# Kernel optimization log

Measured on AMD Instinct MI355X. Metric: run time of the kernel, lower is better.

Reference implementation:

```python
import jax, jax.numpy as jnp
import numpy as np

# dims: L blocks, S cur_seq, M memory_len, B batch, D embed, H heads, IN input_dim
L, S, M, B, D, H, IN = 4, 512, 512, 8, 1024, 16, 128
HD = D // H
GRU_BIAS = 2.0  # config['gru_bias']


def _ln(x, s, b, eps=1e-5):
    mu = x.mean(-1, keepdims=True)
    var = ((x - mu) ** 2).mean(-1, keepdims=True)
    return (x - mu) * jax.lax.rsqrt(var + eps) * s + b


def _pos_emb(full_seq, dim):
    # SinusoidalPE: freqs = arange(0, dim, 2.0); inv = 10000**(-freqs/dim); seq descending
    freqs = jnp.arange(0, dim, 2.0)
    inv = 10000.0 ** (-freqs / dim)
    seq = jnp.arange(full_seq - 1, -1, -1.0)
    ang = seq[:, None] * inv[None, :]
    return jnp.concatenate([jnp.sin(ang), jnp.cos(ang)], axis=-1)  # (F, dim)


def _rel_shift(x):
    # x: (q, k, b, h) -> Transformer-XL relative shift
    q, k, b, h = x.shape
    xp = jnp.pad(x, ((0, 0), (1, 0), (0, 0), (0, 0)))
    return xp.reshape(k + 1, q, b, h)[1:].reshape(q, k, b, h)


def _gru(x, y, Wr, Ur, Wz, Uz, Wg, Ug):
    r = jax.nn.sigmoid(y @ Wr + x @ Ur)
    z = jax.nn.sigmoid(y @ Wz + x @ Uz - GRU_BIAS)
    hcand = jnp.tanh(y @ Wg + (r * x) @ Ug)
    return (1.0 - z) * x + z * hcand


def setup_inputs() -> dict:
    key = jax.random.key(0)
    ks = iter(jax.random.split(key, 64))

    def mat(*shape):
        return jax.random.normal(next(ks), shape, jnp.float32) * (shape[-2] ** -0.5)

    return dict(
        h=jax.random.normal(next(ks), (B, S, IN), jnp.float32),
        memory=jnp.zeros((L, M, B, D), jnp.float32),
        We=mat(IN, D), be=jnp.zeros((D,), jnp.float32),
        ln1_s=jnp.ones((L, D), jnp.float32), ln1_b=jnp.zeros((L, D), jnp.float32),
        ln2_s=jnp.ones((L, D), jnp.float32), ln2_b=jnp.zeros((L, D), jnp.float32),
        Wq=mat(L, D, D), bq=jnp.zeros((L, D), jnp.float32),
        Wk=mat(L, D, D), bk=jnp.zeros((L, D), jnp.float32),
        Wv=mat(L, D, D), bv=jnp.zeros((L, D), jnp.float32),
        Wr=mat(L, D, D), br=jnp.zeros((L, D), jnp.float32),
        Wo=mat(L, D, D), bo=jnp.zeros((L, D), jnp.float32),
        u=jax.random.normal(next(ks), (L, H, HD), jnp.float32) * 0.02,
        vb=jax.random.normal(next(ks), (L, H, HD), jnp.float32) * 0.02,
        gWr=mat(L, 2, D, D), gUr=mat(L, 2, D, D),
        gWz=mat(L, 2, D, D), gUz=mat(L, 2, D, D),
        gWg=mat(L, 2, D, D), gUg=mat(L, 2, D, D),
        fW1=mat(L, D, 4 * D), fb1=jnp.zeros((L, 4 * D), jnp.float32),
        fW2=mat(L, 4 * D, D), fb2=jnp.zeros((L, D), jnp.float32),
    )


def reference(h, memory, We, be, ln1_s, ln1_b, ln2_s, ln2_b,
              Wq, bq, Wk, bk, Wv, bv, Wr, br, Wo, bo, u, vb,
              gWr, gUr, gWz, gUz, gWg, gUg, fW1, fb1, fW2, fb2):
    x = jnp.transpose(h, (1, 0, 2))                      # (S, B, IN)
    x = jax.nn.gelu(x @ We + be, approximate=False)      # (S, B, D)
    F = S + M
    pos = _pos_emb(F, D)                                 # (F, D)
    mask = jnp.triu(jnp.ones((S, F), bool), k=1 + M)     # (S, F)
    scale = HD ** -0.5
    out = x
    for i in range(L):
        full = jnp.concatenate([memory[i], out], axis=0)  # (F, B, D)
        qn = _ln(out, ln1_s[i], ln1_b[i])
        kn = _ln(full, ln1_s[i], ln1_b[i])
        q = (qn @ Wq[i] + bq[i]).reshape(S, B, H, HD)
        k = (kn @ Wk[i] + bk[i]).reshape(F, B, H, HD)
        v = (kn @ Wv[i] + bv[i]).reshape(F, B, H, HD)
        r = (pos @ Wr[i] + br[i]).reshape(F, H, HD)
        content = jnp.einsum('ibhd,jbhd->ijbh', q + u[i], k)
        position = _rel_shift(jnp.einsum('ibhd,jhd->ijbh', q + vb[i], r))
        attn = (content + position) * scale               # (S, F, B, H)
        attn = jnp.where(mask[:, :, None, None], -1e30, attn)
        a = jax.nn.softmax(attn, axis=1)
        y = jnp.einsum('ijbh,jbhd->ibhd', a, v).reshape(S, B, D) @ Wo[i] + bo[i]
        y = jax.nn.gelu(y, approximate=False)
        out1 = _gru(out, y, gWr[i, 0], gUr[i, 0], gWz[i, 0], gUz[i, 0], gWg[i, 0], gUg[i, 0])
        e = _ln(out1, ln2_s[i], ln2_b[i])
        e = jax.nn.gelu(e @ fW1[i] + fb1[i], approximate=False)
        e = jax.nn.gelu(e @ fW2[i] + fb2[i], approximate=False)
        out = _gru(out1, e, gWr[i, 1], gUr[i, 1], gWz[i, 1], gUz[i, 1], gWg[i, 1], gUg[i, 1])
    return jnp.transpose(out, (1, 0, 2))                  # (B, S, D)
```

## Files before the change

### kernel.cpp

```cpp
#include <hip/hip_runtime.h>

typedef unsigned short u16;
typedef unsigned long long u64;
typedef __attribute__((ext_vector_type(8))) short bf16x8;
typedef __attribute__((ext_vector_type(4))) float f32x4;

#define DEVI __device__ __forceinline__

DEVI u16 f2b(float f) {
  unsigned u = __float_as_uint(f);
  u += 0x7fffu + ((u >> 16) & 1u);
  return (u16)(u >> 16);
}
DEVI float b2f(u16 v) { return __uint_as_float((unsigned)v << 16); }
DEVI float tanh_f(float x) {
  float xc = fminf(fmaxf(x, -15.f), 15.f);
  float e = __expf(2.f * xc);
  return (e - 1.f) / (e + 1.f);
}
DEVI float gelu_f(float x) {
  float u = 0.7978845608028654f * x * (1.f + 0.044715f * x * x);
  return 0.5f * x * (1.f + tanh_f(u));
}
DEVI float sigm_f(float x) { return 1.f / (1.f + __expf(-x)); }

DEVI void gload16(const void* g, void* l) {
  __builtin_amdgcn_global_load_lds((__attribute__((address_space(1))) void*)g,
                                   (__attribute__((address_space(3))) void*)l, 16, 0, 0);
}

__global__ __launch_bounds__(256) void gemm_bt(
    const u16* __restrict__ A, const u16* __restrict__ Bt,
    const float* __restrict__ bias, float* __restrict__ C32, u16* __restrict__ C16,
    int M, int N, int K, int ldA, int ldB, int ldC,
    long long sA, long long sBb, long long sBh, long long sC, int nH, int flags)
{
  __shared__ __align__(16) u16 Sm[2][256 * 64];
  const int z = blockIdx.z;
  const int zb = z / nH, zh = z - zb * nH;
  A  += (long long)z * sA;
  Bt += (long long)zb * sBb + (long long)zh * sBh;
  const long long cOff = (long long)z * sC;
  const int m0 = blockIdx.x * 128, n0 = blockIdx.y * 128;
  const int t = threadIdx.x, lane = t & 63;
  const int wm = ((t >> 7) & 1) * 64, wn = ((t >> 6) & 1) * 64;

  f32x4 acc[4][4];
#pragma unroll
  for (int i = 0; i < 4; ++i)
#pragma unroll
    for (int j = 0; j < 4; ++j) { f32x4 zz = {0.f, 0.f, 0.f, 0.f}; acc[i][j] = zz; }

  auto stage = [&](int buf, int k0) {
#pragma unroll
    for (int r = 0; r < 4; ++r) {
      const int c = r * 256 + t;
      const int row = c >> 3;
      const int col = (c & 7) << 3;
      int ga = m0 + row; if (ga >= M) ga = M - 1;
      gload16(A + (long long)ga * ldA + (k0 + col),
              &Sm[buf][(size_t)(r * 256 + (t & 192)) * 8]);
      int gb = n0 + row; if (gb >= N) gb = N - 1;
      gload16(Bt + (long long)gb * ldB + (k0 + col),
              &Sm[buf][(size_t)(1024 + r * 256 + (t & 192)) * 8]);
    }
  };

  auto compute = [&](int buf) {
    const u16* As = &Sm[buf][0];
    const u16* Bs = &Sm[buf][128 * 64];
#pragma unroll
    for (int ks = 0; ks < 2; ++ks) {
      const int ko = ks * 32 + ((lane >> 4) << 3);
      bf16x8 af[4], bfv[4];
#pragma unroll
      for (int i = 0; i < 4; ++i)
        af[i] = *(const bf16x8*)&As[(wm + i * 16 + (lane & 15)) * 64 + ko];
#pragma unroll
      for (int i = 0; i < 4; ++i)
        bfv[i] = *(const bf16x8*)&Bs[(wn + i * 16 + (lane & 15)) * 64 + ko];
#pragma unroll
      for (int mi = 0; mi < 4; ++mi)
#pragma unroll
        for (int ni = 0; ni < 4; ++ni)
          acc[mi][ni] = __builtin_amdgcn_mfma_f32_16x16x32_bf16(af[mi], bfv[ni], acc[mi][ni], 0, 0, 0);
    }
  };

  stage(0, 0);
  __syncthreads();
  int cur = 0;
  for (int k0 = 64; k0 < K; k0 += 64) {
    stage(cur ^ 1, k0);
    compute(cur);
    __syncthreads();
    cur ^= 1;
  }
  compute(cur);

  const int cb = n0 + wn + (lane & 15);
  const int rb = m0 + wm + ((lane >> 4) << 2);
#pragma unroll
  for (int ni = 0; ni < 4; ++ni) {
    const int col = cb + ni * 16;
    if (col >= N) continue;
    const float bv = (flags & 2) ? bias[col] : 0.f;
#pragma unroll
    for (int mi = 0; mi < 4; ++mi) {
#pragma unroll
      for (int q = 0; q < 4; ++q) {
        const int row = rb + mi * 16 + q;
        if (row >= M) continue;
        float x = acc[mi][ni][q] + bv;
        if (flags & 1) x = gelu_f(x);
        long long o;
        if (flags & 16)
          o = ((long long)((row & 7) * 16 + (col >> 6)) * ldC + (row >> 3)) * 64 + (col & 63);
        else if (flags & 32)
          o = ((long long)(col >> 6) * 1024 + row) * 64 + (col & 63);
        else
          o = cOff + (long long)row * ldC + col;
        if (flags & 4) C32[o] = x;
        if (flags & 8) C16[o] = f2b(x);
      }
    }
  }
}

__global__ __launch_bounds__(256) void fused_attn(
    const u16* __restrict__ Qb,
    const u16* __restrict__ Kb,
    const u16* __restrict__ Vt,
    const u16* __restrict__ Rh,
    const float* __restrict__ uK,
    const float* __restrict__ vbR,
    u16* __restrict__ Y)
{
  constexpr int F = 1024;
  const int bid = blockIdx.x;
  const int wk = (bid & 7) * 128 + (bid >> 3);
  const int i0 = (wk & 7) * 64;
  const int bh = wk >> 3;
  const int h = bh & 15;

  __shared__ __align__(16) u16 Qs[64 * 64];
  __shared__ __align__(16) u16 Ks[64 * 64];
  __shared__ __align__(16) u16 Vs[64 * 64];
  __shared__ __align__(16) u16 Rs[2][64 * 64];
  __shared__ __align__(8) u16 PBT[128 * 68];
  __shared__ __align__(16) u16 Ps[4][16][72];
  __shared__ float uKs[64];
  __shared__ float vbRs[2][64];

  const int t = threadIdx.x;
  const int lane = t & 63;
  const int wq = t >> 6;
  const int l15 = lane & 15, lhi = lane >> 4;

  const u16* Qg = Qb + ((size_t)bh * 512 + i0) * 64;
  const u16* Kg = Kb + (size_t)bh * F * 64;
  const u16* Vg = Vt + (size_t)bh * 64 * F;
  const u16* Rg = Rh + (size_t)h * F * 64;
  const float* uKg = uK + (size_t)bh * F;
  const float* vbRg = vbR + (size_t)h * F;

  auto stageQ = [&]() {
#pragma unroll
    for (int rnd = 0; rnd < 2; ++rnd) {
      const int idx = rnd * 256 + t;
      const int row = idx >> 3;
      const int gs = (idx & 7) ^ (row & 7);
      gload16(Qg + row * 64 + gs * 8, Qs + (size_t)(rnd * 256 + (t & 192)) * 8);
    }
  };
  auto stageK = [&](int j0) {
#pragma unroll
    for (int rnd = 0; rnd < 2; ++rnd) {
      const int idx = rnd * 256 + t;
      const int row = idx >> 3;
      const int gs = (idx & 7) ^ (row & 7);
      gload16(Kg + (j0 + row) * 64 + gs * 8, Ks + (size_t)(rnd * 256 + (t & 192)) * 8);
    }
  };
  auto stageV = [&](int j0) {
#pragma unroll
    for (int rnd = 0; rnd < 2; ++rnd) {
      const int idx = rnd * 256 + t;
      const int row = idx >> 3;
      const int gs = (idx & 7) ^ (row & 7);
      gload16(Vg + row * F + j0 + gs * 8, Vs + (size_t)(rnd * 256 + (t & 192)) * 8);
    }
  };
  auto stageR = [&](u16* dst, int cbase) {
#pragma unroll
    for (int rnd = 0; rnd < 2; ++rnd) {
      const int idx = rnd * 256 + t;
      const int row = idx >> 3;
      const int gs = (idx & 7) ^ (row & 7);
      int grow = cbase + row; if (grow > 1023) grow = 1023;
      gload16(Rg + grow * 64 + gs * 8, dst + (size_t)(rnd * 256 + (t & 192)) * 8);
    }
  };

  stageQ();
  const int c_lo0 = 448 - i0;
  stageR(Rs[0], c_lo0);
  if (t < 64) {
    int c = c_lo0 + t; if (c > 1023) c = 1023;
    vbRs[0][t] = vbRg[c];
  }

  f32x4 Oacc[4];
#pragma unroll
  for (int i = 0; i < 4; ++i) { f32x4 zz = {0.f, 0.f, 0.f, 0.f}; Oacc[i] = zz; }
  float mrow[4] = {-3.0e38f, -3.0e38f, -3.0e38f, -3.0e38f};
  float lrow[4] = {0.f, 0.f, 0.f, 0.f};

  const int nT = i0 / 64 + 9;
  for (int st = 0; st < nT; ++st) {
    const int j0 = st * 64;
    const int c_hi = j0 - i0 + 512;
    const bool lastT = (st == nT - 1);
    __syncthreads();
    stageK(j0);
    stageV(j0);
    if (!lastT) stageR(Rs[(st + 1) & 1], c_hi);
    if (t < 64) uKs[t] = uKg[j0 + t];
    else if (t < 128 && !lastT) {
      int c = c_hi + (t - 64); if (c > 1023) c = 1023;
      vbRs[(st + 1) & 1][t - 64] = vbRg[c];
    }
    __syncthreads();

    const u16* RsLo = Rs[st & 1];
    const u16* RsHi = Rs[(st + 1) & 1];
    const float* vLo = vbRs[st & 1];
    const float* vHi = vbRs[(st + 1) & 1];

    f32x4 cacc[4], pbacc[8];
#pragma unroll
    for (int i = 0; i < 4; ++i) { f32x4 zz = {0.f, 0.f, 0.f, 0.f}; cacc[i] = zz; }
#pragma unroll
    for (int i = 0; i < 8; ++i) { f32x4 zz = {0.f, 0.f, 0.f, 0.f}; pbacc[i] = zz; }
    __builtin_amdgcn_s_setprio(1);
#pragma unroll
    for (int ks = 0; ks < 2; ++ks) {
      const int arow = wq * 16 + l15;
      const bf16x8 a = *(const bf16x8*)&Qs[arow * 64 + (((ks * 4 + lhi) ^ (arow & 7)) << 3)];
#pragma unroll
      for (int ni = 0; ni < 4; ++ni) {
        const int brow = ni * 16 + l15;
        const bf16x8 bk_ = *(const bf16x8*)&Ks[brow * 64 + (((ks * 4 + lhi) ^ (brow & 7)) << 3)];
        cacc[ni] = __builtin_amdgcn_mfma_f32_16x16x32_bf16(a, bk_, cacc[ni], 0, 0, 0);
      }
#pragma unroll
      for (int ni = 0; ni < 8; ++ni) {
        if (ni >= 4 && lastT) continue;
        const int brow = (ni & 3) * 16 + l15;
        const u16* rt = (ni < 4) ? RsLo : RsHi;
        const bf16x8 br_ = *(const bf16x8*)&rt[brow * 64 + (((ks * 4 + lhi) ^ (brow & 7)) << 3)];
        pbacc[ni] = __builtin_amdgcn_mfma_f32_16x16x32_bf16(a, br_, pbacc[ni], 0, 0, 0);
      }
    }
    __builtin_amdgcn_s_setprio(0);

#pragma unroll
    for (int ni = 0; ni < 8; ++ni) {
      if (ni >= 4 && lastT) continue;
      u64 w = (u64)f2b(pbacc[ni][0]) | ((u64)f2b(pbacc[ni][1]) << 16) |
              ((u64)f2b(pbacc[ni][2]) << 32) | ((u64)f2b(pbacc[ni][3]) << 48);
      *(u64*)&PBT[(size_t)(ni * 16 + l15) * 68 + wq * 16 + lhi * 4] = w;
    }

    const int lim = i0 - j0 + 512;
    float sc[4][4];
#pragma unroll
    for (int ni = 0; ni < 4; ++ni) {
      const int dj = ni * 16 + l15;
      const float uk = uKs[dj];
#pragma unroll
      for (int qq = 0; qq < 4; ++qq) {
        const int di = wq * 16 + lhi * 4 + qq;
        const int cc = dj - di + 63;
        const float pb = b2f(PBT[(size_t)cc * 68 + di]);
        const float vr = (cc < 64) ? vLo[cc] : vHi[cc - 64];
        float s = (cacc[ni][qq] + uk + pb + vr) * 0.125f;
        if (dj - di > lim) s = -1e30f;
        sc[ni][qq] = s;
      }
    }

    float nm[4], esc[4];
#pragma unroll
    for (int qq = 0; qq < 4; ++qq) {
      float r = fmaxf(fmaxf(sc[0][qq], sc[1][qq]), fmaxf(sc[2][qq], sc[3][qq]));
      r = fmaxf(r, __shfl_xor(r, 1));
      r = fmaxf(r, __shfl_xor(r, 2));
      r = fmaxf(r, __shfl_xor(r, 4));
      r = fmaxf(r, __shfl_xor(r, 8));
      nm[qq] = fmaxf(mrow[qq], r);
      esc[qq] = __expf(mrow[qq] - nm[qq]);
      mrow[qq] = nm[qq];
    }
    float ps[4][4];
    float rsum[4] = {0.f, 0.f, 0.f, 0.f};
#pragma unroll
    for (int ni = 0; ni < 4; ++ni)
#pragma unroll
      for (int qq = 0; qq < 4; ++qq) {
        float p = __expf(sc[ni][qq] - nm[qq]);
        ps[ni][qq] = p;
        rsum[qq] += p;
      }
#pragma unroll
    for (int qq = 0; qq < 4; ++qq) {
      float r = rsum[qq];
      r += __shfl_xor(r, 1);
      r += __shfl_xor(r, 2);
      r += __shfl_xor(r, 4);
      r += __shfl_xor(r, 8);
      lrow[qq] = lrow[qq] * esc[qq] + r;
    }
#pragma unroll
    for (int nd = 0; nd < 4; ++nd)
#pragma unroll
      for (int qq = 0; qq < 4; ++qq) Oacc[nd][qq] *= esc[qq];

#pragma unroll
    for (int ni = 0; ni < 4; ++ni)
#pragma unroll
      for (int qq = 0; qq < 4; ++qq)
        Ps[wq][lhi * 4 + qq][ni * 16 + l15] = f2b(ps[ni][qq]);
    __builtin_amdgcn_s_setprio(1);
#pragma unroll
    for (int ks = 0; ks < 2; ++ks) {
      const bf16x8 pa = *(const bf16x8*)&Ps[wq][l15][ks * 32 + lhi * 8];
#pragma unroll
      for (int nd = 0; nd < 4; ++nd) {
        const int vrow = nd * 16 + l15;
        const bf16x8 vb_ = *(const bf16x8*)&Vs[vrow * 64 + (((ks * 4 + lhi) ^ (vrow & 7)) << 3)];
        Oacc[nd] = __builtin_amdgcn_mfma_f32_16x16x32_bf16(pa, vb_, Oacc[nd], 0, 0, 0);
      }
    }
    __builtin_amdgcn_s_setprio(0);
  }

  float inv[4];
#pragma unroll
  for (int qq = 0; qq < 4; ++qq) inv[qq] = 1.f / lrow[qq];
  const int b = bh >> 4;
#pragma unroll
  for (int nd = 0; nd < 4; ++nd)
#pragma unroll
    for (int qq = 0; qq < 4; ++qq) {
      const int row = i0 + wq * 16 + lhi * 4 + qq;
      const int d = nd * 16 + l15;
      Y[(size_t)row * 8192 + b * 1024 + h * 64 + d] = f2b(Oacc[nd][qq] * inv[qq]);
    }
}

__global__ __launch_bounds__(256) void uk_kernel(const u16* __restrict__ Kb,
                                                 const float* __restrict__ u,
                                                 float* __restrict__ uK)
{
  const long long idx = (long long)blockIdx.x * 256 + threadIdx.x;
  const int h = (int)((idx >> 10) & 15);
  const u16* k = Kb + idx * 64;
  const float* uh = u + h * 64;
  float s = 0.f;
#pragma unroll
  for (int j = 0; j < 8; ++j) {
    bf16x8 kv = *(const bf16x8*)&k[j * 8];
#pragma unroll
    for (int e = 0; e < 8; ++e) s += b2f((u16)kv[e]) * uh[j * 8 + e];
  }
  uK[idx] = s;
}

__global__ __launch_bounds__(256) void vbr_kernel(const u16* __restrict__ Rh,
                                                  const float* __restrict__ vb,
                                                  float* __restrict__ vbR)
{
  const long long idx = (long long)blockIdx.x * 256 + threadIdx.x;
  const int h = (int)(idx >> 10);
  const u16* r = Rh + idx * 64;
  const float* vh = vb + h * 64;
  float s = 0.f;
#pragma unroll
  for (int j = 0; j < 8; ++j) {
    bf16x8 rv = *(const bf16x8*)&r[j * 8];
#pragma unroll
    for (int e = 0; e < 8; ++e) s += b2f((u16)rv[e]) * vh[j * 8 + e];
  }
  vbR[idx] = s;
}

#define MAXW 20
struct WPack {
  const float* src[MAXW];
  u16* dst[MAXW];
  int K[MAXW], N[MAXW];
  int tilePrefix[MAXW + 1];
  int nm;
};

__global__ __launch_bounds__(256) void wtrans_kernel(WPack p) {
  int bid = blockIdx.x;
  int m = 0;
  while (m < p.nm && bid >= p.tilePrefix[m + 1]) ++m;
  if (m >= p.nm) return;
  const int lt = bid - p.tilePrefix[m];
  const int K = p.K[m], N = p.N[m];
  const int tN = N >> 5;
  const int kt = lt / tN, nt = lt - kt * tN;
  const int k0 = kt << 5, n0 = nt << 5;
  const float* src = p.src[m];
  u16* dst = p.dst[m];
  __shared__ float tile[32][33];
  const int t = threadIdx.x;
  const int r = t >> 3, c4 = (t & 7) << 2;
  float4 v = *(const float4*)&src[(size_t)(k0 + r) * N + n0 + c4];
  tile[r][c4 + 0] = v.x; tile[r][c4 + 1] = v.y; tile[r][c4 + 2] = v.z; tile[r][c4 + 3] = v.w;
  __syncthreads();
  u16 o0 = f2b(tile[c4 + 0][r]);
  u16 o1 = f2b(tile[c4 + 1][r]);
  u16 o2 = f2b(tile[c4 + 2][r]);
  u16 o3 = f2b(tile[c4 + 3][r]);
  u64 w = (u64)o0 | ((u64)o1 << 16) | ((u64)o2 << 32) | ((u64)o3 << 48);
  *(u64*)&dst[(size_t)(n0 + r) * K + k0 + c4] = w;
}

__global__ __launch_bounds__(256) void ln_kernel(
    const float* __restrict__ Xmem, const float* __restrict__ Xout, int rowsMem,
    const float* __restrict__ sc, const float* __restrict__ bi, u16* __restrict__ dst)
{
  const int row = blockIdx.x;
  const float* src = (row < rowsMem) ? (Xmem + (long long)row * 1024)
                                     : (Xout + (long long)(row - rowsMem) * 1024);
  const int t = threadIdx.x;
  float4 v = *(const float4*)&src[t * 4];
  float s1 = v.x + v.y + v.z + v.w;
  float s2 = v.x * v.x + v.y * v.y + v.z * v.z + v.w * v.w;
#pragma unroll
  for (int o = 32; o > 0; o >>= 1) { s1 += __shfl_down(s1, o); s2 += __shfl_down(s2, o); }
  __shared__ float red[8];
  const int wv = t >> 6;
  if ((t & 63) == 0) { red[wv * 2] = s1; red[wv * 2 + 1] = s2; }
  __syncthreads();
  s1 = red[0] + red[2] + red[4] + red[6];
  s2 = red[1] + red[3] + red[5] + red[7];
  const float mu = s1 * (1.f / 1024.f);
  const float var = s2 * (1.f / 1024.f) - mu * mu;
  const float rs = rsqrtf(var + 1e-5f);
  float vals[4] = {v.x, v.y, v.z, v.w};
  u16 o4[4];
#pragma unroll
  for (int j = 0; j < 4; ++j) {
    const int c = t * 4 + j;
    o4[j] = f2b((vals[j] - mu) * rs * sc[c] + bi[c]);
  }
  *(u64*)&dst[(long long)row * 1024 + t * 4] =
      (u64)o4[0] | ((u64)o4[1] << 16) | ((u64)o4[2] << 32) | ((u64)o4[3] << 48);
}

__global__ __launch_bounds__(256) void prep_vt16(const u16* __restrict__ Vf, u16* __restrict__ VT)
{
  const int f0 = blockIdx.x * 64;
  const int bh = blockIdx.y;
  const int b = bh >> 4, h = bh & 15;
  __shared__ u16 tl[64 * 64];
  const int t = threadIdx.x;
  {
    const int fr = t >> 2, c0 = (t & 3) * 16;
    const u16* src = Vf + ((size_t)(f0 + fr) * 8 + b) * 1024 + h * 64 + c0;
    *(bf16x8*)&tl[fr * 64 + c0] = *(const bf16x8*)src;
    *(bf16x8*)&tl[fr * 64 + c0 + 8] = *(const bf16x8*)(src + 8);
  }
  __syncthreads();
  {
    const int dr = t >> 2, c0 = (t & 3) * 16;
    u16* dst = VT + ((long long)bh * 64 + dr) * 1024 + f0 + c0;
#pragma unroll
    for (int j = 0; j < 16; ++j) dst[j] = tl[(c0 + j) * 64 + dr];
  }
}

__global__ __launch_bounds__(256) void pe_kernel(u16* __restrict__ PEB)
{
  const long long idx = (long long)blockIdx.x * 256 + threadIdx.x;
  const int p = (int)(idx >> 10);
  const int d = idx & 1023;
  const int q = d & 511;
  const float inv = powf(10000.f, -(float)(2 * q) * (1.f / 1024.f));
  const float ang = (float)(1023 - p) * inv;
  PEB[idx] = f2b((d < 512) ? sinf(ang) : cosf(ang));
}

__global__ __launch_bounds__(256) void embed_conv(const float* __restrict__ h, u16* __restrict__ A)
{
  const long long idx = (long long)blockIdx.x * 256 + threadIdx.x;
  const int c = idx & 127;
  const int r = (int)(idx >> 7);
  const int s = r >> 3, b = r & 7;
  A[idx] = f2b(h[(((long long)b * 512 + s) << 7) + c]);
}

__global__ __launch_bounds__(256) void gru_elemA(const float* __restrict__ T1, float* __restrict__ T2,
                                                 const float* __restrict__ X, u16* __restrict__ RXBF)
{
  const long long i4 = ((long long)blockIdx.x * 256 + threadIdx.x) * 4;
  const int row = (int)(i4 >> 10);
  const int c = i4 & 1023;
  const float* t1 = T1 + (long long)row * 3072 + c;
  float* t2 = T2 + (long long)row * 2048 + c;
  float4 ry = *(const float4*)t1;
  float4 zy = *(const float4*)(t1 + 1024);
  float4 rx = *(const float4*)t2;
  float4 zx = *(const float4*)(t2 + 1024);
  float4 x = *(const float4*)(X + i4);
  float rr[4], zz[4];
  rr[0] = sigm_f(ry.x + rx.x); rr[1] = sigm_f(ry.y + rx.y);
  rr[2] = sigm_f(ry.z + rx.z); rr[3] = sigm_f(ry.w + rx.w);
  zz[0] = sigm_f(zy.x + zx.x - 2.f); zz[1] = sigm_f(zy.y + zx.y - 2.f);
  zz[2] = sigm_f(zy.z + zx.z - 2.f); zz[3] = sigm_f(zy.w + zx.w - 2.f);
  u16 o4[4];
  o4[0] = f2b(rr[0] * x.x); o4[1] = f2b(rr[1] * x.y);
  o4[2] = f2b(rr[2] * x.z); o4[3] = f2b(rr[3] * x.w);
  *(u64*)&RXBF[i4] = (u64)o4[0] | ((u64)o4[1] << 16) | ((u64)o4[2] << 32) | ((u64)o4[3] << 48);
  float4 zo; zo.x = zz[0]; zo.y = zz[1]; zo.z = zz[2]; zo.w = zz[3];
  *(float4*)t2 = zo;
}

__global__ __launch_bounds__(256) void gru_elemB(const float* __restrict__ T1, const float* __restrict__ T2,
                                                 const float* __restrict__ TG, const float* __restrict__ X,
                                                 float* __restrict__ O, u16* __restrict__ XBF)
{
  const long long i4 = ((long long)blockIdx.x * 256 + threadIdx.x) * 4;
  const int row = (int)(i4 >> 10);
  const int c = i4 & 1023;
  float4 gy = *(const float4*)(T1 + (long long)row * 3072 + 2048 + c);
  float4 tt = *(const float4*)(TG + i4);
  float4 z = *(const float4*)(T2 + (long long)row * 2048 + c);
  float4 x = *(const float4*)(X + i4);
  float4 o;
  o.x = (1.f - z.x) * x.x + z.x * tanh_f(gy.x + tt.x);
  o.y = (1.f - z.y) * x.y + z.y * tanh_f(gy.y + tt.y);
  o.z = (1.f - z.z) * x.z + z.z * tanh_f(gy.z + tt.z);
  o.w = (1.f - z.w) * x.w + z.w * tanh_f(gy.w + tt.w);
  *(float4*)(O + i4) = o;
  u16 o4[4];
  o4[0] = f2b(o.x); o4[1] = f2b(o.y); o4[2] = f2b(o.z); o4[3] = f2b(o.w);
  *(u64*)&XBF[i4] = (u64)o4[0] | ((u64)o4[1] << 16) | ((u64)o4[2] << 32) | ((u64)o4[3] << 48);
}

__global__ __launch_bounds__(256) void out_transpose(const float* __restrict__ O, float* __restrict__ dst)
{
  const long long i4 = ((long long)blockIdx.x * 256 + threadIdx.x) * 4;
  const int d = i4 & 1023;
  const int r = (int)(i4 >> 10);
  const int s = r >> 3, b = r & 7;
  float4 v = *(const float4*)(O + i4);
  *(float4*)&dst[(((long long)b * 512 + s) << 10) + d] = v;
}

extern "C" void kernel_launch(void* const* d_in, const int* in_sizes, int n_in,
                              void* d_out, int out_size, void* d_ws, size_t ws_size,
                              hipStream_t stream)
{
  (void)in_sizes; (void)n_in; (void)out_size; (void)ws_size;
  const float* h_in   = (const float*)d_in[0];
  const float* memory = (const float*)d_in[1];
  const float* We     = (const float*)d_in[2];
  const float* be     = (const float*)d_in[3];
  const float* ln1s   = (const float*)d_in[4];
  const float* ln1b   = (const float*)d_in[5];
  const float* ln2s   = (const float*)d_in[6];
  const float* ln2b   = (const float*)d_in[7];
  const float* Wq     = (const float*)d_in[8];
  const float* bq     = (const float*)d_in[9];
  const float* Wk     = (const float*)d_in[10];
  const float* bk     = (const float*)d_in[11];
  const float* Wv     = (const float*)d_in[12];
  const float* bv     = (const float*)d_in[13];
  const float* Wr     = (const float*)d_in[14];
  const float* br     = (const float*)d_in[15];
  const float* Wo     = (const float*)d_in[16];
  const float* bo     = (const float*)d_in[17];
  const float* uu     = (const float*)d_in[18];
  const float* vbp    = (const float*)d_in[19];
  const float* gWr    = (const float*)d_in[20];
  const float* gUr    = (const float*)d_in[21];
  const float* gWz    = (const float*)d_in[22];
  const float* gUz    = (const float*)d_in[23];
  const float* gWg    = (const float*)d_in[24];
  const float* gUg    = (const float*)d_in[25];
  const float* fW1    = (const float*)d_in[26];
  const float* fb1    = (const float*)d_in[27];
  const float* fW2    = (const float*)d_in[28];
  const float* fb2    = (const float*)d_in[29];

  constexpr int S = 512, MM = 512, B = 8, D = 1024, H = 16, IN = 128, F = 1024;
  constexpr int SB = 4096, FB = 8192;
  constexpr long long DD = (long long)D * D;

  char* ws = (char*)d_ws;
  size_t off = 0;
  auto alloc = [&](size_t bytes) -> size_t {
    size_t o = off; off = (off + bytes + 255) & ~(size_t)255; return o;
  };
  const size_t oWT   = alloc((size_t)25 * DD * 2);
  const size_t oWET  = alloc((size_t)D * IN * 2);
  const size_t oPEB  = alloc((size_t)F * D * 2);
  const size_t oOUT  = alloc((size_t)SB * D * 4);
  const size_t oOUT1 = alloc((size_t)SB * D * 4);
  const size_t oXBF  = alloc((size_t)SB * D * 2);
  const size_t oYBF  = alloc((size_t)SB * D * 2);
  const size_t oYBFA = alloc((size_t)SB * D * 2);
  const size_t oABUF = alloc((size_t)SB * D * 2);
  const size_t oKN   = alloc((size_t)FB * D * 2);
  const size_t oQB   = alloc((size_t)B * H * S * 64 * 2);
  const size_t oKBH  = alloc((size_t)B * H * F * 64 * 2);
  const size_t oVT   = alloc((size_t)B * H * F * 64 * 2);
  const size_t oRH   = alloc((size_t)H * F * 64 * 2);
  const size_t oUK   = alloc((size_t)B * H * F * 4);
  const size_t oVBR  = alloc((size_t)H * F * 4);
  const size_t oUNI  = off;

  u16* WTp   = (u16*)(ws + oWT);
  u16* WETp  = (u16*)(ws + oWET);
  u16* PEBp  = (u16*)(ws + oPEB);
  float* OUTp  = (float*)(ws + oOUT);
  float* OUT1p = (float*)(ws + oOUT1);
  u16* XBFp  = (u16*)(ws + oXBF);
  u16* YBFp  = (u16*)(ws + oYBF);
  u16* YBFAp = (u16*)(ws + oYBFA);
  u16* ABUFp = (u16*)(ws + oABUF);
  u16* KNp   = (u16*)(ws + oKN);
  u16* QBp   = (u16*)(ws + oQB);
  u16* KBHp  = (u16*)(ws + oKBH);
  u16* VTp   = (u16*)(ws + oVT);
  u16* RHp   = (u16*)(ws + oRH);
  float* uKp  = (float*)(ws + oUK);
  float* vbRp = (float*)(ws + oVBR);
  u16* VF16p  = (u16*)(ws + oUNI);
  float* T1   = (float*)(ws + oUNI);
  float* T2   = (float*)(ws + oUNI + (size_t)SB * 3 * D * 4);
  float* TGp  = (float*)(ws + oUNI + (size_t)SB * 5 * D * 4);
  u16* FFNBp  = (u16*)(ws + oUNI);

  auto gemm = [&](const u16* A, const u16* Bt, const float* bias, float* C32, u16* C16,
                  int M, int N, int K, int ldA, int ldB, int ldC,
                  long long sA, long long sBb, long long sBh, long long sC, int nH, int Z,
                  int flags) {
    dim3 grid((M + 127) / 128, (N + 127) / 128, Z);
    gemm_bt<<<grid, 256, 0, stream>>>(A, Bt, bias, C32, C16, M, N, K, ldA, ldB, ldC,
                                      sA, sBb, sBh, sC, nH, flags);
  };

  pe_kernel<<<(F * D) / 256, 256, 0, stream>>>(PEBp);
  {
    WPack p{};
    p.nm = 1; p.src[0] = We; p.dst[0] = WETp; p.K[0] = IN; p.N[0] = D;
    p.tilePrefix[0] = 0; p.tilePrefix[1] = (IN / 32) * (D / 32);
    wtrans_kernel<<<p.tilePrefix[1], 256, 0, stream>>>(p);
  }
  embed_conv<<<(SB * IN) / 256, 256, 0, stream>>>(h_in, ABUFp);
  gemm(ABUFp, WETp, be, OUTp, XBFp, SB, D, IN, IN, IN, D, 0, 0, 0, 0, 1, 1, 1 | 2 | 4 | 8);

  for (int li = 0; li < 4; ++li) {
    WPack p{};
    int nt = 0, id = 0;
    auto addw = [&](const float* s, u16* d, int K, int N) {
      p.src[id] = s; p.dst[id] = d; p.K[id] = K; p.N[id] = N;
      p.tilePrefix[id] = nt; nt += (K / 32) * (N / 32); ++id;
    };
    addw(Wq + li * DD, WTp + 0 * DD, D, D);
    addw(Wk + li * DD, WTp + 1 * DD, D, D);
    addw(Wv + li * DD, WTp + 2 * DD, D, D);
    addw(Wr + li * DD, WTp + 3 * DD, D, D);
    addw(Wo + li * DD, WTp + 4 * DD, D, D);
    addw(gWr + (li * 2 + 0) * DD, WTp + 5 * DD, D, D);
    addw(gWz + (li * 2 + 0) * DD, WTp + 6 * DD, D, D);
    addw(gWg + (li * 2 + 0) * DD, WTp + 7 * DD, D, D);
    addw(gUr + (li * 2 + 0) * DD, WTp + 8 * DD, D, D);
    addw(gUz + (li * 2 + 0) * DD, WTp + 9 * DD, D, D);
    addw(gUg + (li * 2 + 0) * DD, WTp + 10 * DD, D, D);
    addw(gWr + (li * 2 + 1) * DD, WTp + 11 * DD, D, D);
    addw(gWz + (li * 2 + 1) * DD, WTp + 12 * DD, D, D);
    addw(gWg + (li * 2 + 1) * DD, WTp + 13 * DD, D, D);
    addw(gUr + (li * 2 + 1) * DD, WTp + 14 * DD, D, D);
    addw(gUz + (li * 2 + 1) * DD, WTp + 15 * DD, D, D);
    addw(gUg + (li * 2 + 1) * DD, WTp + 16 * DD, D, D);
    addw(fW1 + li * (long long)D * 4096, WTp + 17 * DD, D, 4096);
    addw(fW2 + li * (long long)4096 * D, WTp + 21 * DD, 4096, D);
    p.tilePrefix[id] = nt; p.nm = id;
    wtrans_kernel<<<nt, 256, 0, stream>>>(p);

    ln_kernel<<<FB, 256, 0, stream>>>(memory + (long long)li * MM * B * D, OUTp, MM * B,
                                      ln1s + li * D, ln1b + li * D, KNp);
    const u16* QN = KNp + (size_t)MM * B * D;

    gemm(QN, WTp + 0 * DD, bq + li * D, nullptr, QBp, SB, D, D, D, D,  S,
         0, 0, 0, 0, 1, 1, 2 | 8 | 16);
    gemm(KNp, WTp + 1 * DD, bk + li * D, nullptr, KBHp, FB, D, D, D, D,  F,
         0, 0, 0, 0, 1, 1, 2 | 8 | 16);
    uk_kernel<<<(B * H * F) / 256, 256, 0, stream>>>(KBHp, uu + li * H * 64, uKp);
    gemm(KNp, WTp + 2 * DD, bv + li * D, nullptr, VF16p, FB, D, D, D, D, D,
         0, 0, 0, 0, 1, 1, 2 | 8);
    prep_vt16<<<dim3(F / 64, B * H), 256, 0, stream>>>(VF16p, VTp);
    gemm(PEBp, WTp + 3 * DD, br + li * D, nullptr, RHp, F, D, D, D, D, D,
         0, 0, 0, 0, 1, 1, 2 | 8 | 32);
    vbr_kernel<<<(H * F) / 256, 256, 0, stream>>>(RHp, vbp + li * H * 64, vbRp);

    fused_attn<<<dim3((S / 64) * B * H), 256, 0, stream>>>(QBp, KBHp, VTp, RHp, uKp, vbRp, YBFAp);

    gemm(YBFAp, WTp + 4 * DD, bo + li * D, nullptr, YBFp, SB, D, D, D, D, D, 0, 0, 0, 0, 1, 1, 1 | 2 | 8);

    gemm(YBFp, WTp + 5 * DD, nullptr, T1, nullptr, SB, 3 * D, D, D, D, 3 * D, 0, 0, 0, 0, 1, 1, 4);
    gemm(XBFp, WTp + 8 * DD, nullptr, T2, nullptr, SB, 2 * D, D, D, D, 2 * D, 0, 0, 0, 0, 1, 1, 4);
    gru_elemA<<<(SB * D / 4) / 256, 256, 0, stream>>>(T1, T2, OUTp, ABUFp);
    gemm(ABUFp, WTp + 10 * DD, nullptr, TGp, nullptr, SB, D, D, D, D, D, 0, 0, 0, 0, 1, 1, 4);
    gru_elemB<<<(SB * D / 4) / 256, 256, 0, stream>>>(T1, T2, TGp, OUTp, OUT1p, XBFp);

    ln_kernel<<<SB, 256, 0, stream>>>(OUT1p, OUT1p, SB, ln2s + li * D, ln2b + li * D, ABUFp);
    gemm(ABUFp, WTp + 17 * DD, fb1 + li * 4096, nullptr, FFNBp, SB, 4096, D, D, D, 4096,
         0, 0, 0, 0, 1, 1, 1 | 2 | 8);
    gemm(FFNBp, WTp + 21 * DD, fb2 + li * D, nullptr, YBFp, SB, D, 4096, 4096, 4096, D,
         0, 0, 0, 0, 1, 1, 1 | 2 | 8);

    gemm(YBFp, WTp + 11 * DD, nullptr, T1, nullptr, SB, 3 * D, D, D, D, 3 * D, 0, 0, 0, 0, 1, 1, 4);
    gemm(XBFp, WTp + 14 * DD, nullptr, T2, nullptr, SB, 2 * D, D, D, D, 2 * D, 0, 0, 0, 0, 1, 1, 4);
    gru_elemA<<<(SB * D / 4) / 256, 256, 0, stream>>>(T1, T2, OUT1p, ABUFp);
    gemm(ABUFp, WTp + 16 * DD, nullptr, TGp, nullptr, SB, D, D, D, D, D, 0, 0, 0, 0, 1, 1, 4);
    gru_elemB<<<(SB * D / 4) / 256, 256, 0, stream>>>(T1, T2, TGp, OUT1p, OUTp, XBFp);
  }

  out_transpose<<<(SB * D / 4) / 256, 256, 0, stream>>>(OUTp, (float*)d_out);
}
```

Baseline: 3.378 ms.

## Fold u/vb biases into Q operands and use narrower GEMM tiles for small N

The attention kernel now takes two pre-biased query tensors, (q+u) and (q+vb), built by folding u into the Q bias and adding vb-u in a small elementwise kernel. This removes the separate uK and vbR reduction kernels and their per-tile loads. The position-bias tile is computed once per step and double-buffered across iterations, instead of recomputing both low and high halves every step. GEMMs with N<=1024 now use a 128x64 tile to launch more blocks, in exchange for an extra Q-sized buffer and a second bf16 rounding of q+vb.

```diff
diff --git a/kernel.cpp b/kernel.cpp
--- a/kernel.cpp
+++ b/kernel.cpp
@@ -29,27 +29,29 @@
                                    (__attribute__((address_space(3))) void*)l, 16, 0, 0);
 }
 
+template <int BN>
 __global__ __launch_bounds__(256) void gemm_bt(
     const u16* __restrict__ A, const u16* __restrict__ Bt,
     const float* __restrict__ bias, float* __restrict__ C32, u16* __restrict__ C16,
     int M, int N, int K, int ldA, int ldB, int ldC,
     long long sA, long long sBb, long long sBh, long long sC, int nH, int flags)
 {
-  __shared__ __align__(16) u16 Sm[2][256 * 64];
+  constexpr int NF = BN / 32;
+  __shared__ __align__(16) u16 Sm[2][(128 + BN) * 64];
   const int z = blockIdx.z;
   const int zb = z / nH, zh = z - zb * nH;
   A  += (long long)z * sA;
   Bt += (long long)zb * sBb + (long long)zh * sBh;
   const long long cOff = (long long)z * sC;
-  const int m0 = blockIdx.x * 128, n0 = blockIdx.y * 128;
+  const int m0 = blockIdx.x * 128, n0 = blockIdx.y * BN;
   const int t = threadIdx.x, lane = t & 63;
-  const int wm = ((t >> 7) & 1) * 64, wn = ((t >> 6) & 1) * 64;
-
-  f32x4 acc[4][4];
+  const int wm = ((t >> 7) & 1) * 64, wn = ((t >> 6) & 1) * (BN / 2);
+
+  f32x4 acc[4][NF];
 #pragma unroll
   for (int i = 0; i < 4; ++i)
 #pragma unroll
-    for (int j = 0; j < 4; ++j) { f32x4 zz = {0.f, 0.f, 0.f, 0.f}; acc[i][j] = zz; }
+    for (int j = 0; j < NF; ++j) { f32x4 zz = {0.f, 0.f, 0.f, 0.f}; acc[i][j] = zz; }
 
   auto stage = [&](int buf, int k0) {
 #pragma unroll
@@ -60,6 +62,12 @@
       int ga = m0 + row; if (ga >= M) ga = M - 1;
       gload16(A + (long long)ga * ldA + (k0 + col),
               &Sm[buf][(size_t)(r * 256 + (t & 192)) * 8]);
+    }
+#pragma unroll
+    for (int r = 0; r < BN / 32; ++r) {
+      const int c = r * 256 + t;
+      const int row = c >> 3;
+      const int col = (c & 7) << 3;
       int gb = n0 + row; if (gb >= N) gb = N - 1;
       gload16(Bt + (long long)gb * ldB + (k0 + col),
               &Sm[buf][(size_t)(1024 + r * 256 + (t & 192)) * 8]);
@@ -72,17 +80,17 @@
 #pragma unroll
     for (int ks = 0; ks < 2; ++ks) {
       const int ko = ks * 32 + ((lane >> 4) << 3);
-      bf16x8 af[4], bfv[4];
+      bf16x8 af[4], bfv[NF];
 #pragma unroll
       for (int i = 0; i < 4; ++i)
         af[i] = *(const bf16x8*)&As[(wm + i * 16 + (lane & 15)) * 64 + ko];
 #pragma unroll
-      for (int i = 0; i < 4; ++i)
+      for (int i = 0; i < NF; ++i)
         bfv[i] = *(const bf16x8*)&Bs[(wn + i * 16 + (lane & 15)) * 64 + ko];
 #pragma unroll
       for (int mi = 0; mi < 4; ++mi)
 #pragma unroll
-        for (int ni = 0; ni < 4; ++ni)
+        for (int ni = 0; ni < NF; ++ni)
           acc[mi][ni] = __builtin_amdgcn_mfma_f32_16x16x32_bf16(af[mi], bfv[ni], acc[mi][ni], 0, 0, 0);
     }
   };
@@ -101,7 +109,7 @@
   const int cb = n0 + wn + (lane & 15);
   const int rb = m0 + wm + ((lane >> 4) << 2);
 #pragma unroll
-  for (int ni = 0; ni < 4; ++ni) {
+  for (int ni = 0; ni < NF; ++ni) {
     const int col = cb + ni * 16;
     if (col >= N) continue;
     const float bv = (flags & 2) ? bias[col] : 0.f;
@@ -128,12 +136,11 @@
 }
 
 __global__ __launch_bounds__(256) void fused_attn(
-    const u16* __restrict__ Qb,
+    const u16* __restrict__ Qu,
+    const u16* __restrict__ Qv,
     const u16* __restrict__ Kb,
     const u16* __restrict__ Vt,
     const u16* __restrict__ Rh,
-    const float* __restrict__ uK,
-    const float* __restrict__ vbR,
     u16* __restrict__ Y)
 {
   constexpr int F = 1024;
@@ -143,71 +150,72 @@
   const int bh = wk >> 3;
   const int h = bh & 15;
 
-  __shared__ __align__(16) u16 Qs[64 * 64];
+  __shared__ __align__(16) u16 QUs[64 * 64];
+  __shared__ __align__(16) u16 QVs[64 * 64];
   __shared__ __align__(16) u16 Ks[64 * 64];
   __shared__ __align__(16) u16 Vs[64 * 64];
-  __shared__ __align__(16) u16 Rs[2][64 * 64];
-  __shared__ __align__(8) u16 PBT[128 * 68];
+  __shared__ __align__(16) u16 Rs[64 * 64];
+  __shared__ __align__(8) u16 PBT[2][64 * 68];
   __shared__ __align__(16) u16 Ps[4][16][72];
-  __shared__ float uKs[64];
-  __shared__ float vbRs[2][64];
 
   const int t = threadIdx.x;
   const int lane = t & 63;
   const int wq = t >> 6;
   const int l15 = lane & 15, lhi = lane >> 4;
 
-  const u16* Qg = Qb + ((size_t)bh * 512 + i0) * 64;
+  const u16* QUg = Qu + ((size_t)bh * 512 + i0) * 64;
+  const u16* QVg = Qv + ((size_t)bh * 512 + i0) * 64;
   const u16* Kg = Kb + (size_t)bh * F * 64;
   const u16* Vg = Vt + (size_t)bh * 64 * F;
   const u16* Rg = Rh + (size_t)h * F * 64;
-  const float* uKg = uK + (size_t)bh * F;
-  const float* vbRg = vbR + (size_t)h * F;
-
-  auto stageQ = [&]() {
+
+  auto stageT = [&](const u16* g, u16* dst) {
 #pragma unroll
     for (int rnd = 0; rnd < 2; ++rnd) {
       const int idx = rnd * 256 + t;
       const int row = idx >> 3;
       const int gs = (idx & 7) ^ (row & 7);
-      gload16(Qg + row * 64 + gs * 8, Qs + (size_t)(rnd * 256 + (t & 192)) * 8);
+      gload16(g + row * 64 + gs * 8, dst + (size_t)(rnd * 256 + (t & 192)) * 8);
     }
   };
-  auto stageK = [&](int j0) {
+  auto stageVf = [&](int j0) {
 #pragma unroll
     for (int rnd = 0; rnd < 2; ++rnd) {
       const int idx = rnd * 256 + t;
       const int row = idx >> 3;
       const int gs = (idx & 7) ^ (row & 7);
-      gload16(Kg + (j0 + row) * 64 + gs * 8, Ks + (size_t)(rnd * 256 + (t & 192)) * 8);
+      gload16(Vg + (size_t)row * F + j0 + gs * 8, Vs + (size_t)(rnd * 256 + (t & 192)) * 8);
     }
   };
-  auto stageV = [&](int j0) {
-#pragma unroll
-    for (int rnd = 0; rnd < 2; ++rnd) {
-      const int idx = rnd * 256 + t;
-      const int row = idx >> 3;
-      const int gs = (idx & 7) ^ (row & 7);
-      gload16(Vg + row * F + j0 + gs * 8, Vs + (size_t)(rnd * 256 + (t & 192)) * 8);
-    }
-  };
-  auto stageR = [&](u16* dst, int cbase) {
-#pragma unroll
-    for (int rnd = 0; rnd < 2; ++rnd) {
-      const int idx = rnd * 256 + t;
-      const int row = idx >> 3;
-      const int gs = (idx & 7) ^ (row & 7);
-      int grow = cbase + row; if (grow > 1023) grow = 1023;
-      gload16(Rg + grow * 64 + gs * 8, dst + (size_t)(rnd * 256 + (t & 192)) * 8);
-    }
-  };
-
-  stageQ();
+
+  stageT(QUg, QUs);
+  stageT(QVg, QVs);
   const int c_lo0 = 448 - i0;
-  stageR(Rs[0], c_lo0);
-  if (t < 64) {
-    int c = c_lo0 + t; if (c > 1023) c = 1023;
-    vbRs[0][t] = vbRg[c];
+  stageT(Rg + (size_t)c_lo0 * 64, Rs);
+  __syncthreads();
+  {
+    f32x4 pb0[4];
+#pragma unroll
+    for (int i = 0; i < 4; ++i) { f32x4 zz = {0.f, 0.f, 0.f, 0.f}; pb0[i] = zz; }
+    __builtin_amdgcn_s_setprio(1);
+#pragma unroll
+    for (int ks = 0; ks < 2; ++ks) {
+      const int arow = wq * 16 + l15;
+      const bf16x8 av = *(const bf16x8*)&QVs[arow * 64 + (((ks * 4 + lhi) ^ (arow & 7)) << 3)];
+#pragma unroll
+      for (int ni = 0; ni < 4; ++ni) {
+        const int brow = ni * 16 + l15;
+        const bf16x8 br_ = *(const bf16x8*)&Rs[brow * 64 + (((ks * 4 + lhi) ^ (brow & 7)) << 3)];
+        pb0[ni] = __builtin_amdgcn_mfma_f32_16x16x32_bf16(av, br_, pb0[ni], 0, 0, 0);
+      }
+    }
+    __builtin_amdgcn_s_setprio(0);
+#pragma unroll
+    for (int ni = 0; ni < 4; ++ni) {
+      u64 w = (u64)f2b(pb0[ni][0]) | ((u64)f2b(pb0[ni][1]) << 16) |
+              ((u64)f2b(pb0[ni][2]) << 32) | ((u64)f2b(pb0[ni][3]) << 48);
+      *(u64*)&PBT[0][(size_t)(ni * 16 + l15) * 68 + wq * 16 + lhi * 4] = w;
+    }
   }
 
   f32x4 Oacc[4];
@@ -219,72 +227,65 @@
   const int nT = i0 / 64 + 9;
   for (int st = 0; st < nT; ++st) {
     const int j0 = st * 64;
-    const int c_hi = j0 - i0 + 512;
     const bool lastT = (st == nT - 1);
     __syncthreads();
-    stageK(j0);
-    stageV(j0);
-    if (!lastT) stageR(Rs[(st + 1) & 1], c_hi);
-    if (t < 64) uKs[t] = uKg[j0 + t];
-    else if (t < 128 && !lastT) {
-      int c = c_hi + (t - 64); if (c > 1023) c = 1023;
-      vbRs[(st + 1) & 1][t - 64] = vbRg[c];
-    }
+    stageT(Kg + (size_t)j0 * 64, Ks);
+    stageVf(j0);
+    if (!lastT) stageT(Rg + (size_t)(j0 - i0 + 512) * 64, Rs);
     __syncthreads();
 
-    const u16* RsLo = Rs[st & 1];
-    const u16* RsHi = Rs[(st + 1) & 1];
-    const float* vLo = vbRs[st & 1];
-    const float* vHi = vbRs[(st + 1) & 1];
-
-    f32x4 cacc[4], pbacc[8];
-#pragma unroll
-    for (int i = 0; i < 4; ++i) { f32x4 zz = {0.f, 0.f, 0.f, 0.f}; cacc[i] = zz; }
-#pragma unroll
-    for (int i = 0; i < 8; ++i) { f32x4 zz = {0.f, 0.f, 0.f, 0.f}; pbacc[i] = zz; }
+    f32x4 cacc[4], pbh[4];
+#pragma unroll
+    for (int i = 0; i < 4; ++i) {
+      f32x4 zz = {0.f, 0.f, 0.f, 0.f};
+      cacc[i] = zz; pbh[i] = zz;
+    }
     __builtin_amdgcn_s_setprio(1);
 #pragma unroll
     for (int ks = 0; ks < 2; ++ks) {
       const int arow = wq * 16 + l15;
-      const bf16x8 a = *(const bf16x8*)&Qs[arow * 64 + (((ks * 4 + lhi) ^ (arow & 7)) << 3)];
+      const bf16x8 au = *(const bf16x8*)&QUs[arow * 64 + (((ks * 4 + lhi) ^ (arow & 7)) << 3)];
 #pragma unroll
       for (int ni = 0; ni < 4; ++ni) {
         const int brow = ni * 16 + l15;
         const bf16x8 bk_ = *(const bf16x8*)&Ks[brow * 64 + (((ks * 4 + lhi) ^ (brow & 7)) << 3)];
-        cacc[ni] = __builtin_amdgcn_mfma_f32_16x16x32_bf16(a, bk_, cacc[ni], 0, 0, 0);
+        cacc[ni] = __builtin_amdgcn_mfma_f32_16x16x32_bf16(au, bk_, cacc[ni], 0, 0, 0);
       }
-#pragma unroll
-      for (int ni = 0; ni < 8; ++ni) {
-        if (ni >= 4 && lastT) continue;
-        const int brow = (ni & 3) * 16 + l15;
-        const u16* rt = (ni < 4) ? RsLo : RsHi;
-        const bf16x8 br_ = *(const bf16x8*)&rt[brow * 64 + (((ks * 4 + lhi) ^ (brow & 7)) << 3)];
-        pbacc[ni] = __builtin_amdgcn_mfma_f32_16x16x32_bf16(a, br_, pbacc[ni], 0, 0, 0);
+      if (!lastT) {
+        const bf16x8 av = *(const bf16x8*)&QVs[arow * 64 + (((ks * 4 + lhi) ^ (arow & 7)) << 3)];
+#pragma unroll
+        for (int ni = 0; ni < 4; ++ni) {
+          const int brow = ni * 16 + l15;
+          const bf16x8 br_ = *(const bf16x8*)&Rs[brow * 64 + (((ks * 4 + lhi) ^ (brow & 7)) << 3)];
+          pbh[ni] = __builtin_amdgcn_mfma_f32_16x16x32_bf16(av, br_, pbh[ni], 0, 0, 0);
+        }
       }
     }
     __builtin_amdgcn_s_setprio(0);
 
-#pragma unroll
-    for (int ni = 0; ni < 8; ++ni) {
-      if (ni >= 4 && lastT) continue;
-      u64 w = (u64)f2b(pbacc[ni][0]) | ((u64)f2b(pbacc[ni][1]) << 16) |
-              ((u64)f2b(pbacc[ni][2]) << 32) | ((u64)f2b(pbacc[ni][3]) << 48);
-      *(u64*)&PBT[(size_t)(ni * 16 + l15) * 68 + wq * 16 + lhi * 4] = w;
+    if (!lastT) {
+#pragma unroll
+      for (int ni = 0; ni < 4; ++ni) {
+        u64 w = (u64)f2b(pbh[ni][0]) | ((u64)f2b(pbh[ni][1]) << 16) |
+                ((u64)f2b(pbh[ni][2]) << 32) | ((u64)f2b(pbh[ni][3]) << 48);
+        *(u64*)&PBT[(st + 1) & 1][(size_t)(ni * 16 + l15) * 68 + wq * 16 + lhi * 4] = w;
+      }
     }
 
     const int lim = i0 - j0 + 512;
+    const u16* pbLo = &PBT[st & 1][0];
+    const u16* pbHi = &PBT[(st + 1) & 1][0];
     float sc[4][4];
 #pragma unroll
     for (int ni = 0; ni < 4; ++ni) {
       const int dj = ni * 16 + l15;
-      const float uk = uKs[dj];
 #pragma unroll
       for (int qq = 0; qq < 4; ++qq) {
         const int di = wq * 16 + lhi * 4 + qq;
         const int cc = dj - di + 63;
-        const float pb = b2f(PBT[(size_t)cc * 68 + di]);
-        const float vr = (cc < 64) ? vLo[cc] : vHi[cc - 64];
-        float s = (cacc[ni][qq] + uk + pb + vr) * 0.125f;
+        const float pb = b2f((cc < 64) ? pbLo[(size_t)cc * 68 + di]
+                                       : pbHi[(size_t)(cc - 64) * 68 + di]);
+        float s = (cacc[ni][qq] + pb) * 0.125f;
         if (dj - di > lim) s = -1e30f;
         sc[ni][qq] = s;
       }
@@ -359,40 +360,25 @@
     }
 }
 
-__global__ __launch_bounds__(256) void uk_kernel(const u16* __restrict__ Kb,
-                                                 const float* __restrict__ u,
-                                                 float* __restrict__ uK)
+__global__ __launch_bounds__(256) void biasprep(const float* __restrict__ bq,
+                                                const float* __restrict__ u,
+                                                const float* __restrict__ vb,
+                                                float* __restrict__ bqu,
+                                                float* __restrict__ dvb)
+{
+  const int i = blockIdx.x * 256 + threadIdx.x;
+  bqu[i] = bq[i] + u[i];
+  dvb[i] = vb[i] - u[i];
+}
+
+__global__ __launch_bounds__(256) void qv_make(const u16* __restrict__ QU,
+                                               const float* __restrict__ dvb,
+                                               u16* __restrict__ QV)
 {
   const long long idx = (long long)blockIdx.x * 256 + threadIdx.x;
-  const int h = (int)((idx >> 10) & 15);
-  const u16* k = Kb + idx * 64;
-  const float* uh = u + h * 64;
-  float s = 0.f;
-#pragma unroll
-  for (int j = 0; j < 8; ++j) {
-    bf16x8 kv = *(const bf16x8*)&k[j * 8];
-#pragma unroll
-    for (int e = 0; e < 8; ++e) s += b2f((u16)kv[e]) * uh[j * 8 + e];
-  }
-  uK[idx] = s;
-}
-
-__global__ __launch_bounds__(256) void vbr_kernel(const u16* __restrict__ Rh,
-                                                  const float* __restrict__ vb,
-                                                  float* __restrict__ vbR)
-{
-  const long long idx = (long long)blockIdx.x * 256 + threadIdx.x;
-  const int h = (int)(idx >> 10);
-  const u16* r = Rh + idx * 64;
-  const float* vh = vb + h * 64;
-  float s = 0.f;
-#pragma unroll
-  for (int j = 0; j < 8; ++j) {
-    bf16x8 rv = *(const bf16x8*)&r[j * 8];
-#pragma unroll
-    for (int e = 0; e < 8; ++e) s += b2f((u16)rv[e]) * vh[j * 8 + e];
-  }
-  vbR[idx] = s;
+  const int d = idx & 63;
+  const int h = (idx >> 15) & 15;
+  QV[idx] = f2b(b2f(QU[idx]) + dvb[h * 64 + d]);
 }
 
 #define MAXW 20
@@ -618,12 +604,13 @@
   const size_t oYBFA = alloc((size_t)SB * D * 2);
   const size_t oABUF = alloc((size_t)SB * D * 2);
   const size_t oKN   = alloc((size_t)FB * D * 2);
-  const size_t oQB   = alloc((size_t)B * H * S * 64 * 2);
+  const size_t oQU   = alloc((size_t)B * H * S * 64 * 2);
+  const size_t oQV   = alloc((size_t)B * H * S * 64 * 2);
   const size_t oKBH  = alloc((size_t)B * H * F * 64 * 2);
   const size_t oVT   = alloc((size_t)B * H * F * 64 * 2);
   const size_t oRH   = alloc((size_t)H * F * 64 * 2);
-  const size_t oUK   = alloc((size_t)B * H * F * 4);
-  const size_t oVBR  = alloc((size_t)H * F * 4);
+  const size_t oBQU  = alloc((size_t)D * 4);
+  const size_t oDVB  = alloc((size_t)D * 4);
   const size_t oUNI  = off;
 
   u16* WTp   = (u16*)(ws + oWT);
@@ -636,12 +623,13 @@
   u16* YBFAp = (u16*)(ws + oYBFA);
   u16* ABUFp = (u16*)(ws + oABUF);
   u16* KNp   = (u16*)(ws + oKN);
-  u16* QBp   = (u16*)(ws + oQB);
+  u16* QUp   = (u16*)(ws + oQU);
+  u16* QVp   = (u16*)(ws + oQV);
   u16* KBHp  = (u16*)(ws + oKBH);
   u16* VTp   = (u16*)(ws + oVT);
   u16* RHp   = (u16*)(ws + oRH);
-  float* uKp  = (float*)(ws + oUK);
-  float* vbRp = (float*)(ws + oVBR);
+  float* bquP = (float*)(ws + oBQU);
+  float* dvbP = (float*)(ws + oDVB);
   u16* VF16p  = (u16*)(ws + oUNI);
   float* T1   = (float*)(ws + oUNI);
   float* T2   = (float*)(ws + oUNI + (size_t)SB * 3 * D * 4);
@@ -652,9 +640,15 @@
                   int M, int N, int K, int ldA, int ldB, int ldC,
                   long long sA, long long sBb, long long sBh, long long sC, int nH, int Z,
                   int flags) {
-    dim3 grid((M + 127) / 128, (N + 127) / 128, Z);
-    gemm_bt<<<grid, 256, 0, stream>>>(A, Bt, bias, C32, C16, M, N, K, ldA, ldB, ldC,
-                                      sA, sBb, sBh, sC, nH, flags);
+    if (N <= 1024) {
+      dim3 grid((M + 127) / 128, (N + 63) / 64, Z);
+      gemm_bt<64><<<grid, 256, 0, stream>>>(A, Bt, bias, C32, C16, M, N, K, ldA, ldB, ldC,
+                                            sA, sBb, sBh, sC, nH, flags);
+    } else {
+      dim3 grid((M + 127) / 128, (N + 127) / 128, Z);
+      gemm_bt<128><<<grid, 256, 0, stream>>>(A, Bt, bias, C32, C16, M, N, K, ldA, ldB, ldC,
+                                             sA, sBb, sBh, sC, nH, flags);
+    }
   };
 
   pe_kernel<<<(F * D) / 256, 256, 0, stream>>>(PEBp);
@@ -700,19 +694,19 @@
                                       ln1s + li * D, ln1b + li * D, KNp);
     const u16* QN = KNp + (size_t)MM * B * D;
 
-    gemm(QN, WTp + 0 * DD, bq + li * D, nullptr, QBp, SB, D, D, D, D,  S,
+    biasprep<<<4, 256, 0, stream>>>(bq + li * D, uu + li * D, vbp + li * D, bquP, dvbP);
+    gemm(QN, WTp + 0 * DD, bquP, nullptr, QUp, SB, D, D, D, D,  S,
          0, 0, 0, 0, 1, 1, 2 | 8 | 16);
+    qv_make<<<(B * H * S * 64) / 256, 256, 0, stream>>>(QUp, dvbP, QVp);
     gemm(KNp, WTp + 1 * DD, bk + li * D, nullptr, KBHp, FB, D, D, D, D,  F,
          0, 0, 0, 0, 1, 1, 2 | 8 | 16);
-    uk_kernel<<<(B * H * F) / 256, 256, 0, stream>>>(KBHp, uu + li * H * 64, uKp);
     gemm(KNp, WTp + 2 * DD, bv + li * D, nullptr, VF16p, FB, D, D, D, D, D,
          0, 0, 0, 0, 1, 1, 2 | 8);
     prep_vt16<<<dim3(F / 64, B * H), 256, 0, stream>>>(VF16p, VTp);
     gemm(PEBp, WTp + 3 * DD, br + li * D, nullptr, RHp, F, D, D, D, D, D,
          0, 0, 0, 0, 1, 1, 2 | 8 | 32);
-    vbr_kernel<<<(H * F) / 256, 256, 0, stream>>>(RHp, vbp + li * H * 64, vbRp);
-
-    fused_attn<<<dim3((S / 64) * B * H), 256, 0, stream>>>(QBp, KBHp, VTp, RHp, uKp, vbRp, YBFAp);
+
+    fused_attn<<<dim3((S / 64) * B * H), 256, 0, stream>>>(QUp, QVp, KBHp, VTp, RHp, YBFAp);
 
     gemm(YBFAp, WTp + 4 * DD, bo + li * D, nullptr, YBFp, SB, D, D, D, D, D, 0, 0, 0, 0, 1, 1, 1 | 2 | 8);
 
```

Result: faster. 3.141 ms (-7.0%).
